# Optimization experiments

Hardware: AMD Instinct MI355X
Metric: run time of the kernel (lower is better)

Reference implementation:

```python
import jax, jax.numpy as jnp
import numpy as np

DECAY = 0.9
BETA_OBS = 1.0
BETA_STATE = 1.0

N_OBS = 20000
N_STATES = 1024
N_ACTIONS = 64
STATE_DIM = 256
RFD = 2048


def setup_inputs() -> dict:
    key = jax.random.key(0)
    ks = jax.random.split(key, 7)
    Q = jax.random.normal(ks[0], (STATE_DIM, N_STATES), dtype=jnp.float32) / np.sqrt(STATE_DIM).astype(np.float32)
    V = jax.random.normal(ks[1], (STATE_DIM, N_ACTIONS), dtype=jnp.float32) / np.sqrt(STATE_DIM).astype(np.float32)
    W = jax.random.normal(ks[2], (RFD, STATE_DIM), dtype=jnp.float32)
    M_re = jax.random.normal(ks[3], (RFD, N_OBS), dtype=jnp.float32)
    M_im = jax.random.normal(ks[4], (RFD, N_OBS), dtype=jnp.float32)
    obs = jax.random.uniform(ks[5], (N_OBS,), dtype=jnp.float32)
    action = jax.random.uniform(ks[6], (N_ACTIONS,), dtype=jnp.float32)
    return {"Q": Q, "V": V, "W": W, "M_re": M_re, "M_im": M_im, "obs": obs, "action": action}


def reference(Q, V, W, M_re, M_im, obs, action):
    # One fused POCML step: memory write (decayed outer product), state
    # rotation via complex random-feature phase, clean_up (state-kernel
    # softmax retrieval), and obs retrieval from memory.
    D = W.shape[0]  # random_feature_dim
    M = M_re + 1j * M_im                       # [D, n_obs] complex64
    obs_c = obs.astype(jnp.complex64)
    # get_state_from_memory
    state0 = M @ obs_c                         # [D]
    # update_memory: M *= decay; M += outer(state, obs)
    M_new = DECAY * M + jnp.outer(state0, obs_c)
    # update_state: v = V @ action; phi_v = exp(1j * W @ v); state *= phi_v
    v = V @ action                             # [state_dim]
    phi_v = jnp.exp(1j * (W @ v))              # [D] complex64
    state1 = state0 * phi_v
    # clean_up: phi_Q = exp(1j * W @ Q), weights = softmax(beta*sim(phi_Q.T, state))
    phi_Q = jnp.exp(1j * (W @ Q))              # [D, n_states]
    score = BETA_STATE * (phi_Q.T @ jnp.conj(state1)).real / D  # [n_states]
    weights = jax.nn.softmax(score)
    state2 = phi_Q @ weights.astype(jnp.complex64)              # [D]
    # get_obs_from_memory: softmax(beta_obs * sim(M.T, state))
    obs_score = BETA_OBS * (M_new.T @ jnp.conj(state2)).real / D  # [n_obs]
    return jax.nn.softmax(obs_score)
```

## Files before the change

kernel.cpp:

```cpp
#include <hip/hip_runtime.h>
#include <math.h>

#define N_OBS    20000
#define N_OBS4   5000
#define N_OBS8   2500
#define N_STATES 1024
#define N_ACT    64
#define SDIM     256
#define RFD      2048
#define DECAY    0.9f
#define NSEG     5
#define SEG_O8   500

typedef float v4f __attribute__((ext_vector_type(4)));
typedef float v2f __attribute__((ext_vector_type(2)));

__device__ __forceinline__ v4f ntload4(const float* p) {
    return __builtin_nontemporal_load((const v4f*)p);
}

__device__ __forceinline__ unsigned pk4_fp8(float a, float b, float c, float d) {
    unsigned w = __builtin_amdgcn_cvt_pk_fp8_f32(a, b, 0u, false);
    w = __builtin_amdgcn_cvt_pk_fp8_f32(c, d, w, true);
    return w;
}

#define OFF_SCORE  0
#define OFF_OBSACC 1024
#define ZERO_CNT   (OFF_OBSACC + N_OBS)
#define OFF_P0RE   21024
#define OFF_P0IM   (OFF_P0RE + NSEG*RFD)
#define OFF_S2RE   (OFF_P0IM + NSEG*RFD)
#define OFF_S2IM   (OFF_S2RE + RFD)
#define OFF_WTS    (OFF_S2IM + RFD)
#define OFF_VWS    (OFF_WTS + N_STATES)
#define OFF_COSQ   (OFF_VWS + SDIM)
#define OFF_SINQ   (OFF_COSQ + RFD*N_STATES)
#define OFF_MH8    (OFF_SINQ + RFD*N_STATES)
#define MH8_FLOATS (RFD * N_OBS8 * 4)
#define WS_FLOATS  (OFF_MH8 + MH8_FLOATS)

#define NB_P1     (RFD * NSEG)
#define NB_GEMM   512
#define NB_FUSED  (NB_P1 + 1 + NB_GEMM)

__global__ __launch_bounds__(256) void k_fused(
    const float* __restrict__ Mre, const float* __restrict__ Mim,
    const float* __restrict__ obs,
    const float* __restrict__ W, const float* __restrict__ Q,
    const float* __restrict__ V, const float* __restrict__ action,
    float* __restrict__ cosQ, float* __restrict__ sinQ,
    float* __restrict__ p0re, float* __restrict__ p0im,
    float* __restrict__ vout, uint4* __restrict__ Mh8)
{
    const int b = blockIdx.x;
    const int tid = threadIdx.x;

    if (b < NB_P1) {
        const int d = b / NSEG;
        const int seg = b - d * NSEG;
        const float* mr = Mre + (size_t)d * N_OBS;
        const float* mi = Mim + (size_t)d * N_OBS;
        uint4* mh = Mh8 + (size_t)d * N_OBS8;
        const float4* ob = (const float4*)obs;
        const int i0 = seg * SEG_O8;
        float ar0 = 0.f, ai0 = 0.f, ar1 = 0.f, ai1 = 0.f;
        {
            int i = i0 + tid;
            float4 oa = ob[2*i], obv = ob[2*i + 1];
            v4f ra = ntload4(mr + 8 * (size_t)i);
            v4f rb = ntload4(mr + 8 * (size_t)i + 4);
            v4f qa = ntload4(mi + 8 * (size_t)i);
            v4f qb = ntload4(mi + 8 * (size_t)i + 4);
            uint4 u;
            u.x = pk4_fp8(ra.x, qa.x, ra.y, qa.y);
            u.y = pk4_fp8(ra.z, qa.z, ra.w, qa.w);
            u.z = pk4_fp8(rb.x, qb.x, rb.y, qb.y);
            u.w = pk4_fp8(rb.z, qb.z, rb.w, qb.w);
            mh[i] = u;
            ar0 += ra.x*oa.x + ra.y*oa.y + ra.z*oa.z + ra.w*oa.w;
            ar1 += rb.x*obv.x + rb.y*obv.y + rb.z*obv.z + rb.w*obv.w;
            ai0 += qa.x*oa.x + qa.y*oa.y + qa.z*oa.z + qa.w*oa.w;
            ai1 += qb.x*obv.x + qb.y*obv.y + qb.z*obv.z + qb.w*obv.w;
        }
        if (tid < SEG_O8 - 256) {
            int i = i0 + 256 + tid;
            float4 oa = ob[2*i], obv = ob[2*i + 1];
            v4f ra = ntload4(mr + 8 * (size_t)i);
            v4f rb = ntload4(mr + 8 * (size_t)i + 4);
            v4f qa = ntload4(mi + 8 * (size_t)i);
            v4f qb = ntload4(mi + 8 * (size_t)i + 4);
            uint4 u;
            u.x = pk4_fp8(ra.x, qa.x, ra.y, qa.y);
            u.y = pk4_fp8(ra.z, qa.z, ra.w, qa.w);
            u.z = pk4_fp8(rb.x, qb.x, rb.y, qb.y);
            u.w = pk4_fp8(rb.z, qb.z, rb.w, qb.w);
            mh[i] = u;
            ar0 += ra.x*oa.x + ra.y*oa.y + ra.z*oa.z + ra.w*oa.w;
            ar1 += rb.x*obv.x + rb.y*obv.y + rb.z*obv.z + rb.w*obv.w;
            ai0 += qa.x*oa.x + qa.y*oa.y + qa.z*oa.z + qa.w*oa.w;
            ai1 += qb.x*obv.x + qb.y*obv.y + qb.z*obv.z + qb.w*obv.w;
        }
        float arr = ar0 + ar1;
        float aii = ai0 + ai1;
        #pragma unroll
        for (int off = 32; off > 0; off >>= 1) {
            arr += __shfl_down(arr, off);
            aii += __shfl_down(aii, off);
        }
        __shared__ float pr[4], pi[4];
        const int wave = tid >> 6, lane = tid & 63;
        if (lane == 0) { pr[wave] = arr; pi[wave] = aii; }
        __syncthreads();
        if (tid == 0) {
            p0re[seg * RFD + d] = pr[0] + pr[1] + pr[2] + pr[3];
            p0im[seg * RFD + d] = pi[0] + pi[1] + pi[2] + pi[3];
        }
    } else if (b == NB_P1) {
        float acc = 0.f;
        for (int a = 0; a < N_ACT; a++) acc += V[tid * N_ACT + a] * action[a];
        vout[tid] = acc;
    } else {
        const int g = b - (NB_P1 + 1);
        __shared__ float As[16][65];
        __shared__ float Bs[16][64];
        const int tx = tid & 15;
        const int ty = tid >> 4;
        const int m0 = (g >> 4) * 64;
        const int n0 = (g & 15) * 64;
        float c[4][4] = {};
        for (int k0 = 0; k0 < SDIM; k0 += 16) {
            {
                int k = tid & 15, mb = tid >> 4;
                #pragma unroll
                for (int j = 0; j < 4; j++)
                    As[k][mb + 16*j] = W[(size_t)(m0 + mb + 16*j) * SDIM + k0 + k];
            }
            {
                int n = tid & 63, kb = tid >> 6;
                #pragma unroll
                for (int j = 0; j < 4; j++)
                    Bs[kb + 4*j][n] = Q[(size_t)(k0 + kb + 4*j) * N_STATES + n0 + n];
            }
            __syncthreads();
            #pragma unroll
            for (int kk = 0; kk < 16; kk++) {
                float a[4], bb[4];
                #pragma unroll
                for (int i = 0; i < 4; i++) a[i] = As[kk][ty*4 + i];
                #pragma unroll
                for (int j = 0; j < 4; j++) bb[j] = Bs[kk][tx*4 + j];
                #pragma unroll
                for (int i = 0; i < 4; i++)
                    #pragma unroll
                    for (int j = 0; j < 4; j++)
                        c[i][j] += a[i] * bb[j];
            }
            __syncthreads();
        }
        #pragma unroll
        for (int i = 0; i < 4; i++) {
            int d = m0 + ty*4 + i;
            #pragma unroll
            for (int j = 0; j < 4; j++) {
                int s = n0 + tx*4 + j;
                float sn, cs;
                sincosf(c[i][j], &sn, &cs);
                cosQ[(size_t)d * N_STATES + s] = cs;
                sinQ[(size_t)d * N_STATES + s] = sn;
            }
        }
    }
}

__global__ __launch_bounds__(256) void k_score(
    const float* __restrict__ cosQ, const float* __restrict__ sinQ,
    const float* __restrict__ W, const float* __restrict__ vws,
    const float* __restrict__ p0re, const float* __restrict__ p0im,
    float* __restrict__ score)
{
    __shared__ float s1r_s[32], s1i_s[32];
    const int tid = threadIdx.x;
    const int d0 = blockIdx.y * 32;
    {
        const int r = tid >> 3, g = tid & 7;
        const float4* wv4 = (const float4*)(W + (size_t)(d0 + r) * SDIM + g * 32);
        const float4* vv4 = (const float4*)(vws + g * 32);
        float th = 0.f;
        #pragma unroll
        for (int j = 0; j < 8; j++) {
            float4 wv = wv4[j], vv = vv4[j];
            th += wv.x*vv.x + wv.y*vv.y + wv.z*vv.z + wv.w*vv.w;
        }
        th += __shfl_xor(th, 4);
        th += __shfl_xor(th, 2);
        th += __shfl_xor(th, 1);
        if (g == 0) {
            const int d = d0 + r;
            float re = 0.f, im = 0.f;
            #pragma unroll
            for (int s = 0; s < NSEG; s++) {
                re += p0re[s * RFD + d];
                im += p0im[s * RFD + d];
            }
            float sn, cs;
            sincosf(th, &sn, &cs);
            s1r_s[r] = re * cs - im * sn;
            s1i_s[r] = re * sn + im * cs;
        }
    }
    __syncthreads();
    const int s = blockIdx.x * 256 + tid;
    float acc = 0.f;
    #pragma unroll 4
    for (int j = 0; j < 32; j++) {
        int d = d0 + j;
        acc += cosQ[(size_t)d * N_STATES + s] * s1r_s[j]
             + sinQ[(size_t)d * N_STATES + s] * s1i_s[j];
    }
    atomicAdd(&score[s], acc);
}

__global__ __launch_bounds__(256) void k_softmax_w(
    const float* __restrict__ score, float* __restrict__ wts)
{
    __shared__ float red[256];
    const int tid = threadIdx.x;
    const float scale = 1.f / (float)RFD;
    float4 v = ((const float4*)score)[tid];
    v.x *= scale; v.y *= scale; v.z *= scale; v.w *= scale;
    float mx = fmaxf(fmaxf(v.x, v.y), fmaxf(v.z, v.w));
    red[tid] = mx; __syncthreads();
    for (int s = 128; s > 0; s >>= 1) {
        if (tid < s) red[tid] = fmaxf(red[tid], red[tid+s]);
        __syncthreads();
    }
    mx = red[0]; __syncthreads();
    float4 e;
    e.x = expf(v.x - mx); e.y = expf(v.y - mx);
    e.z = expf(v.z - mx); e.w = expf(v.w - mx);
    red[tid] = e.x + e.y + e.z + e.w; __syncthreads();
    for (int s = 128; s > 0; s >>= 1) {
        if (tid < s) red[tid] += red[tid+s];
        __syncthreads();
    }
    const float inv = 1.f / red[0];
    e.x *= inv; e.y *= inv; e.z *= inv; e.w *= inv;
    ((float4*)wts)[tid] = e;
}

__global__ __launch_bounds__(256) void k_state2(
    const float* __restrict__ cosQ, const float* __restrict__ sinQ,
    const float* __restrict__ wts,
    float* __restrict__ s2re, float* __restrict__ s2im)
{
    __shared__ float r1[256], r2[256];
    const int d = blockIdx.x, tid = threadIdx.x;
    float4 w = ((const float4*)wts)[tid];
    float4 a = ((const float4*)(cosQ + (size_t)d * N_STATES))[tid];
    float4 b = ((const float4*)(sinQ + (size_t)d * N_STATES))[tid];
    r1[tid] = a.x*w.x + a.y*w.y + a.z*w.z + a.w*w.w;
    r2[tid] = b.x*w.x + b.y*w.y + b.z*w.z + b.w*w.w;
    __syncthreads();
    for (int s = 128; s > 0; s >>= 1) {
        if (tid < s) { r1[tid] += r1[tid+s]; r2[tid] += r2[tid+s]; }
        __syncthreads();
    }
    if (tid == 0) { s2re[d] = r1[0]; s2im[d] = r2[0]; }
}

__global__ __launch_bounds__(256) void k_obs_acc8(
    const uint4* __restrict__ Mh8,
    const float* __restrict__ s2re, const float* __restrict__ s2im,
    float* __restrict__ obs_acc)
{
    __shared__ float c_s[32], s_s[32];
    const int tid = threadIdx.x;
    const int dbase = blockIdx.y * 32;
    if (tid < 32) { c_s[tid] = s2re[dbase + tid]; s_s[tid] = s2im[dbase + tid]; }
    __syncthreads();
    const int idx = blockIdx.x * 256 + tid;
    if (idx >= N_OBS8) return;
    const uint4* p = Mh8 + (size_t)dbase * N_OBS8 + idx;
    float a0 = 0.f, a1 = 0.f, a2 = 0.f, a3 = 0.f;
    float a4 = 0.f, a5 = 0.f, a6 = 0.f, a7 = 0.f;
    #pragma unroll 4
    for (int j = 0; j < 32; ++j) {
        uint4 u = p[(size_t)j * N_OBS8];
        float cc = c_s[j], ss = s_s[j];
        v2f f0 = __builtin_amdgcn_cvt_pk_f32_fp8(u.x, false);
        v2f f1 = __builtin_amdgcn_cvt_pk_f32_fp8(u.x, true);
        v2f f2 = __builtin_amdgcn_cvt_pk_f32_fp8(u.y, false);
        v2f f3 = __builtin_amdgcn_cvt_pk_f32_fp8(u.y, true);
        v2f f4 = __builtin_amdgcn_cvt_pk_f32_fp8(u.z, false);
        v2f f5 = __builtin_amdgcn_cvt_pk_f32_fp8(u.z, true);
        v2f f6 = __builtin_amdgcn_cvt_pk_f32_fp8(u.w, false);
        v2f f7 = __builtin_amdgcn_cvt_pk_f32_fp8(u.w, true);
        a0 += f0.x*cc + f0.y*ss;
        a1 += f1.x*cc + f1.y*ss;
        a2 += f2.x*cc + f2.y*ss;
        a3 += f3.x*cc + f3.y*ss;
        a4 += f4.x*cc + f4.y*ss;
        a5 += f5.x*cc + f5.y*ss;
        a6 += f6.x*cc + f6.y*ss;
        a7 += f7.x*cc + f7.y*ss;
    }
    float* dst = obs_acc + idx * 8;
    atomicAdd(dst + 0, a0);
    atomicAdd(dst + 1, a1);
    atomicAdd(dst + 2, a2);
    atomicAdd(dst + 3, a3);
    atomicAdd(dst + 4, a4);
    atomicAdd(dst + 5, a5);
    atomicAdd(dst + 6, a6);
    atomicAdd(dst + 7, a7);
}

__global__ __launch_bounds__(1024) void k_softmax_obs(
    const float* __restrict__ obs_acc, const float* __restrict__ obs,
    const float* __restrict__ p0re, const float* __restrict__ p0im,
    const float* __restrict__ s2re, const float* __restrict__ s2im,
    float* __restrict__ out)
{
    __shared__ float red[1024];
    const int tid = threadIdx.x;
    float dp = 0.f;
    #pragma unroll
    for (int i = 0; i < 2; i++) {
        int d = tid + i * 1024;
        float re = 0.f, im = 0.f;
        #pragma unroll
        for (int s = 0; s < NSEG; s++) {
            re += p0re[s * RFD + d];
            im += p0im[s * RFD + d];
        }
        dp += re * s2re[d] + im * s2im[d];
    }
    red[tid] = dp; __syncthreads();
    for (int s = 512; s > 0; s >>= 1) {
        if (tid < s) red[tid] += red[tid+s];
        __syncthreads();
    }
    const float d0 = red[0];
    __syncthreads();
    const float scale = 1.f / (float)RFD;
    float vals[20];
    float mx = -3.402823466e+38f;
    #pragma unroll
    for (int i = 0; i < 20; i++) {
        int idx = tid + i * 1024;
        if (idx < N_OBS) {
            float sc = (DECAY * obs_acc[idx] + obs[idx] * d0) * scale;
            vals[i] = sc;
            mx = fmaxf(mx, sc);
        } else vals[i] = -3.402823466e+38f;
    }
    red[tid] = mx; __syncthreads();
    for (int s = 512; s > 0; s >>= 1) {
        if (tid < s) red[tid] = fmaxf(red[tid], red[tid+s]);
        __syncthreads();
    }
    mx = red[0]; __syncthreads();
    float sum = 0.f;
    #pragma unroll
    for (int i = 0; i < 20; i++) {
        int idx = tid + i * 1024;
        if (idx < N_OBS) {
            vals[i] = expf(vals[i] - mx);
            sum += vals[i];
        }
    }
    red[tid] = sum; __syncthreads();
    for (int s = 512; s > 0; s >>= 1) {
        if (tid < s) red[tid] += red[tid+s];
        __syncthreads();
    }
    const float inv = 1.f / red[0];
    #pragma unroll
    for (int i = 0; i < 20; i++) {
        int idx = tid + i * 1024;
        if (idx < N_OBS) out[idx] = vals[i] * inv;
    }
}

extern "C" void kernel_launch(void* const* d_in, const int* in_sizes, int n_in,
                              void* d_out, int out_size, void* d_ws, size_t ws_size,
                              hipStream_t stream) {
    const float* Q      = (const float*)d_in[0];
    const float* V      = (const float*)d_in[1];
    const float* W      = (const float*)d_in[2];
    const float* Mre    = (const float*)d_in[3];
    const float* Mim    = (const float*)d_in[4];
    const float* obs    = (const float*)d_in[5];
    const float* action = (const float*)d_in[6];
    float* out = (float*)d_out;
    float* ws  = (float*)d_ws;

    if (ws_size < (size_t)WS_FLOATS * sizeof(float)) return;

    float* score = ws + OFF_SCORE;
    float* oacc  = ws + OFF_OBSACC;
    float* p0re  = ws + OFF_P0RE;
    float* p0im  = ws + OFF_P0IM;
    float* s2re  = ws + OFF_S2RE;
    float* s2im  = ws + OFF_S2IM;
    float* wts   = ws + OFF_WTS;
    float* vws   = ws + OFF_VWS;
    float* cosQ  = ws + OFF_COSQ;
    float* sinQ  = ws + OFF_SINQ;
    uint4* Mh8   = (uint4*)(ws + OFF_MH8);

    hipMemsetAsync(ws, 0, (size_t)ZERO_CNT * sizeof(float), stream);

    k_fused<<<NB_FUSED, 256, 0, stream>>>(Mre, Mim, obs, W, Q, V, action,
                                          cosQ, sinQ, p0re, p0im, vws, Mh8);
    k_score<<<dim3(4, 64), 256, 0, stream>>>(cosQ, sinQ, W, vws, p0re, p0im, score);
    k_softmax_w<<<1, 256, 0, stream>>>(score, wts);
    k_state2<<<RFD, 256, 0, stream>>>(cosQ, sinQ, wts, s2re, s2im);
    k_obs_acc8<<<dim3(10, 64), 256, 0, stream>>>(Mh8, s2re, s2im, oacc);
    k_softmax_obs<<<1, 1024, 0, stream>>>(oacc, obs, p0re, p0im, s2re, s2im, out);
}
```

Measured before the change: 444.4 us.

## Fuse softmax into state2, fold memset into fused kernel, reorder block roles

Moves workspace zeroing from a separate memset into extra blocks of the first fused kernel. The GEMM blocks are scheduled first, and the M streaming pass is split into two halves per row instead of five segments. The softmax over state scores is merged into the state2 kernel, which each block recomputes redundantly, and that kernel also reduces the state0·state2 dot product via an atomic. The aim is to save launches and the final kernel's reduction, at the cost of redundant softmax work in 1024 blocks.

```diff
diff --git a/kernel.cpp b/kernel.cpp
--- a/kernel.cpp
+++ b/kernel.cpp
@@ -2,15 +2,14 @@
 #include <math.h>
 
 #define N_OBS    20000
-#define N_OBS4   5000
 #define N_OBS8   2500
 #define N_STATES 1024
 #define N_ACT    64
 #define SDIM     256
 #define RFD      2048
 #define DECAY    0.9f
-#define NSEG     5
-#define SEG_O8   500
+#define HALF_O8  1250
+#define FLTMAX   3.402823466e+38f
 
 typedef float v4f __attribute__((ext_vector_type(4)));
 typedef float v2f __attribute__((ext_vector_type(2)));
@@ -27,22 +26,23 @@
 
 #define OFF_SCORE  0
 #define OFF_OBSACC 1024
-#define ZERO_CNT   (OFF_OBSACC + N_OBS)
-#define OFF_P0RE   21024
-#define OFF_P0IM   (OFF_P0RE + NSEG*RFD)
-#define OFF_S2RE   (OFF_P0IM + NSEG*RFD)
+#define OFF_DOT0   21024
+#define ZERO_CNT   21028
+#define OFF_P0RE   21028
+#define OFF_P0IM   (OFF_P0RE + 2*RFD)
+#define OFF_S2RE   (OFF_P0IM + 2*RFD)
 #define OFF_S2IM   (OFF_S2RE + RFD)
-#define OFF_WTS    (OFF_S2IM + RFD)
-#define OFF_VWS    (OFF_WTS + N_STATES)
+#define OFF_VWS    (OFF_S2IM + RFD)
 #define OFF_COSQ   (OFF_VWS + SDIM)
 #define OFF_SINQ   (OFF_COSQ + RFD*N_STATES)
 #define OFF_MH8    (OFF_SINQ + RFD*N_STATES)
 #define MH8_FLOATS (RFD * N_OBS8 * 4)
 #define WS_FLOATS  (OFF_MH8 + MH8_FLOATS)
 
-#define NB_P1     (RFD * NSEG)
 #define NB_GEMM   512
-#define NB_FUSED  (NB_P1 + 1 + NB_GEMM)
+#define NB_Z      21
+#define NB_P1     (RFD * 2)
+#define NB_FUSED  (NB_GEMM + 1 + NB_Z + NB_P1)
 
 __global__ __launch_bounds__(256) void k_fused(
     const float* __restrict__ Mre, const float* __restrict__ Mim,
@@ -51,83 +51,19 @@
     const float* __restrict__ V, const float* __restrict__ action,
     float* __restrict__ cosQ, float* __restrict__ sinQ,
     float* __restrict__ p0re, float* __restrict__ p0im,
-    float* __restrict__ vout, uint4* __restrict__ Mh8)
+    float* __restrict__ vout, uint4* __restrict__ Mh8,
+    float* __restrict__ zbase)
 {
     const int b = blockIdx.x;
     const int tid = threadIdx.x;
 
-    if (b < NB_P1) {
-        const int d = b / NSEG;
-        const int seg = b - d * NSEG;
-        const float* mr = Mre + (size_t)d * N_OBS;
-        const float* mi = Mim + (size_t)d * N_OBS;
-        uint4* mh = Mh8 + (size_t)d * N_OBS8;
-        const float4* ob = (const float4*)obs;
-        const int i0 = seg * SEG_O8;
-        float ar0 = 0.f, ai0 = 0.f, ar1 = 0.f, ai1 = 0.f;
-        {
-            int i = i0 + tid;
-            float4 oa = ob[2*i], obv = ob[2*i + 1];
-            v4f ra = ntload4(mr + 8 * (size_t)i);
-            v4f rb = ntload4(mr + 8 * (size_t)i + 4);
-            v4f qa = ntload4(mi + 8 * (size_t)i);
-            v4f qb = ntload4(mi + 8 * (size_t)i + 4);
-            uint4 u;
-            u.x = pk4_fp8(ra.x, qa.x, ra.y, qa.y);
-            u.y = pk4_fp8(ra.z, qa.z, ra.w, qa.w);
-            u.z = pk4_fp8(rb.x, qb.x, rb.y, qb.y);
-            u.w = pk4_fp8(rb.z, qb.z, rb.w, qb.w);
-            mh[i] = u;
-            ar0 += ra.x*oa.x + ra.y*oa.y + ra.z*oa.z + ra.w*oa.w;
-            ar1 += rb.x*obv.x + rb.y*obv.y + rb.z*obv.z + rb.w*obv.w;
-            ai0 += qa.x*oa.x + qa.y*oa.y + qa.z*oa.z + qa.w*oa.w;
-            ai1 += qb.x*obv.x + qb.y*obv.y + qb.z*obv.z + qb.w*obv.w;
-        }
-        if (tid < SEG_O8 - 256) {
-            int i = i0 + 256 + tid;
-            float4 oa = ob[2*i], obv = ob[2*i + 1];
-            v4f ra = ntload4(mr + 8 * (size_t)i);
-            v4f rb = ntload4(mr + 8 * (size_t)i + 4);
-            v4f qa = ntload4(mi + 8 * (size_t)i);
-            v4f qb = ntload4(mi + 8 * (size_t)i + 4);
-            uint4 u;
-            u.x = pk4_fp8(ra.x, qa.x, ra.y, qa.y);
-            u.y = pk4_fp8(ra.z, qa.z, ra.w, qa.w);
-            u.z = pk4_fp8(rb.x, qb.x, rb.y, qb.y);
-            u.w = pk4_fp8(rb.z, qb.z, rb.w, qb.w);
-            mh[i] = u;
-            ar0 += ra.x*oa.x + ra.y*oa.y + ra.z*oa.z + ra.w*oa.w;
-            ar1 += rb.x*obv.x + rb.y*obv.y + rb.z*obv.z + rb.w*obv.w;
-            ai0 += qa.x*oa.x + qa.y*oa.y + qa.z*oa.z + qa.w*oa.w;
-            ai1 += qb.x*obv.x + qb.y*obv.y + qb.z*obv.z + qb.w*obv.w;
-        }
-        float arr = ar0 + ar1;
-        float aii = ai0 + ai1;
-        #pragma unroll
-        for (int off = 32; off > 0; off >>= 1) {
-            arr += __shfl_down(arr, off);
-            aii += __shfl_down(aii, off);
-        }
-        __shared__ float pr[4], pi[4];
-        const int wave = tid >> 6, lane = tid & 63;
-        if (lane == 0) { pr[wave] = arr; pi[wave] = aii; }
-        __syncthreads();
-        if (tid == 0) {
-            p0re[seg * RFD + d] = pr[0] + pr[1] + pr[2] + pr[3];
-            p0im[seg * RFD + d] = pi[0] + pi[1] + pi[2] + pi[3];
-        }
-    } else if (b == NB_P1) {
-        float acc = 0.f;
-        for (int a = 0; a < N_ACT; a++) acc += V[tid * N_ACT + a] * action[a];
-        vout[tid] = acc;
-    } else {
-        const int g = b - (NB_P1 + 1);
+    if (b < NB_GEMM) {
         __shared__ float As[16][65];
         __shared__ float Bs[16][64];
         const int tx = tid & 15;
         const int ty = tid >> 4;
-        const int m0 = (g >> 4) * 64;
-        const int n0 = (g & 15) * 64;
+        const int m0 = (b >> 4) * 64;
+        const int n0 = (b & 15) * 64;
         float c[4][4] = {};
         for (int k0 = 0; k0 < SDIM; k0 += 16) {
             {
@@ -170,6 +106,61 @@
                 sinQ[(size_t)d * N_STATES + s] = sn;
             }
         }
+    } else if (b == NB_GEMM) {
+        float acc = 0.f;
+        for (int a = 0; a < N_ACT; a++) acc += V[tid * N_ACT + a] * action[a];
+        vout[tid] = acc;
+    } else if (b < NB_GEMM + 1 + NB_Z) {
+        int idx = (b - (NB_GEMM + 1)) * 256 + tid;
+        if (idx < ZERO_CNT / 4)
+            ((float4*)zbase)[idx] = make_float4(0.f, 0.f, 0.f, 0.f);
+    } else {
+        const int p = b - (NB_GEMM + 1 + NB_Z);
+        const int d = p >> 1;
+        const int h = p & 1;
+        const float* mr = Mre + (size_t)d * N_OBS;
+        const float* mi = Mim + (size_t)d * N_OBS;
+        uint4* mh = Mh8 + (size_t)d * N_OBS8;
+        const float4* ob = (const float4*)obs;
+        const int base = h * HALF_O8, lim = base + HALF_O8;
+        float ar0 = 0.f, ar1 = 0.f, ai0 = 0.f, ai1 = 0.f;
+        int i = base + tid;
+        #pragma unroll
+        for (int it = 0; it < 5; ++it, i += 256) {
+            int ic = i < lim ? i : lim - 1;
+            float4 oa = ob[2*ic], obv = ob[2*ic + 1];
+            v4f ra = ntload4(mr + 8 * (size_t)ic);
+            v4f rb = ntload4(mr + 8 * (size_t)ic + 4);
+            v4f qa = ntload4(mi + 8 * (size_t)ic);
+            v4f qb = ntload4(mi + 8 * (size_t)ic + 4);
+            if (i < lim) {
+                uint4 u;
+                u.x = pk4_fp8(ra.x, qa.x, ra.y, qa.y);
+                u.y = pk4_fp8(ra.z, qa.z, ra.w, qa.w);
+                u.z = pk4_fp8(rb.x, qb.x, rb.y, qb.y);
+                u.w = pk4_fp8(rb.z, qb.z, rb.w, qb.w);
+                mh[ic] = u;
+                ar0 += ra.x*oa.x + ra.y*oa.y + ra.z*oa.z + ra.w*oa.w;
+                ar1 += rb.x*obv.x + rb.y*obv.y + rb.z*obv.z + rb.w*obv.w;
+                ai0 += qa.x*oa.x + qa.y*oa.y + qa.z*oa.z + qa.w*oa.w;
+                ai1 += qb.x*obv.x + qb.y*obv.y + qb.z*obv.z + qb.w*obv.w;
+            }
+        }
+        float arr = ar0 + ar1;
+        float aii = ai0 + ai1;
+        #pragma unroll
+        for (int off = 32; off > 0; off >>= 1) {
+            arr += __shfl_down(arr, off);
+            aii += __shfl_down(aii, off);
+        }
+        __shared__ float pr[4], pi[4];
+        const int wave = tid >> 6, lane = tid & 63;
+        if (lane == 0) { pr[wave] = arr; pi[wave] = aii; }
+        __syncthreads();
+        if (tid == 0) {
+            p0re[h * RFD + d] = pr[0] + pr[1] + pr[2] + pr[3];
+            p0im[h * RFD + d] = pi[0] + pi[1] + pi[2] + pi[3];
+        }
     }
 }
 
@@ -197,12 +188,8 @@
         th += __shfl_xor(th, 1);
         if (g == 0) {
             const int d = d0 + r;
-            float re = 0.f, im = 0.f;
-            #pragma unroll
-            for (int s = 0; s < NSEG; s++) {
-                re += p0re[s * RFD + d];
-                im += p0im[s * RFD + d];
-            }
+            float re = p0re[d] + p0re[RFD + d];
+            float im = p0im[d] + p0im[RFD + d];
             float sn, cs;
             sincosf(th, &sn, &cs);
             s1r_s[r] = re * cs - im * sn;
@@ -221,10 +208,16 @@
     atomicAdd(&score[s], acc);
 }
 
-__global__ __launch_bounds__(256) void k_softmax_w(
-    const float* __restrict__ score, float* __restrict__ wts)
+__global__ __launch_bounds__(256) void k_wst2(
+    const float* __restrict__ cosQ, const float* __restrict__ sinQ,
+    const float* __restrict__ score,
+    const float* __restrict__ p0re, const float* __restrict__ p0im,
+    float* __restrict__ s2re, float* __restrict__ s2im,
+    float* __restrict__ dot0)
 {
     __shared__ float red[256];
+    __shared__ float r1[256], r2[256];
+    const int b = blockIdx.x;
     const int tid = threadIdx.x;
     const float scale = 1.f / (float)RFD;
     float4 v = ((const float4*)score)[tid];
@@ -246,27 +239,29 @@
     }
     const float inv = 1.f / red[0];
     e.x *= inv; e.y *= inv; e.z *= inv; e.w *= inv;
-    ((float4*)wts)[tid] = e;
-}
-
-__global__ __launch_bounds__(256) void k_state2(
-    const float* __restrict__ cosQ, const float* __restrict__ sinQ,
-    const float* __restrict__ wts,
-    float* __restrict__ s2re, float* __restrict__ s2im)
-{
-    __shared__ float r1[256], r2[256];
-    const int d = blockIdx.x, tid = threadIdx.x;
-    float4 w = ((const float4*)wts)[tid];
-    float4 a = ((const float4*)(cosQ + (size_t)d * N_STATES))[tid];
-    float4 b = ((const float4*)(sinQ + (size_t)d * N_STATES))[tid];
-    r1[tid] = a.x*w.x + a.y*w.y + a.z*w.z + a.w*w.w;
-    r2[tid] = b.x*w.x + b.y*w.y + b.z*w.z + b.w*w.w;
     __syncthreads();
-    for (int s = 128; s > 0; s >>= 1) {
-        if (tid < s) { r1[tid] += r1[tid+s]; r2[tid] += r2[tid+s]; }
-        __syncthreads();
-    }
-    if (tid == 0) { s2re[d] = r1[0]; s2im[d] = r2[0]; }
+    float blockdot = 0.f;
+    #pragma unroll
+    for (int r = 0; r < 2; r++) {
+        const int d = b * 2 + r;
+        float4 a = ((const float4*)(cosQ + (size_t)d * N_STATES))[tid];
+        float4 bb = ((const float4*)(sinQ + (size_t)d * N_STATES))[tid];
+        r1[tid] = a.x*e.x + a.y*e.y + a.z*e.z + a.w*e.w;
+        r2[tid] = bb.x*e.x + bb.y*e.y + bb.z*e.z + bb.w*e.w;
+        __syncthreads();
+        for (int s = 128; s > 0; s >>= 1) {
+            if (tid < s) { r1[tid] += r1[tid+s]; r2[tid] += r2[tid+s]; }
+            __syncthreads();
+        }
+        if (tid == 0) {
+            s2re[d] = r1[0]; s2im[d] = r2[0];
+            float s0r = p0re[d] + p0re[RFD + d];
+            float s0i = p0im[d] + p0im[RFD + d];
+            blockdot += s0r * r1[0] + s0i * r2[0];
+        }
+        __syncthreads();
+    }
+    if (tid == 0) atomicAdd(dot0, blockdot);
 }
 
 __global__ __launch_bounds__(256) void k_obs_acc8(
@@ -318,34 +313,15 @@
 
 __global__ __launch_bounds__(1024) void k_softmax_obs(
     const float* __restrict__ obs_acc, const float* __restrict__ obs,
-    const float* __restrict__ p0re, const float* __restrict__ p0im,
-    const float* __restrict__ s2re, const float* __restrict__ s2im,
+    const float* __restrict__ dot0,
     float* __restrict__ out)
 {
     __shared__ float red[1024];
     const int tid = threadIdx.x;
-    float dp = 0.f;
-    #pragma unroll
-    for (int i = 0; i < 2; i++) {
-        int d = tid + i * 1024;
-        float re = 0.f, im = 0.f;
-        #pragma unroll
-        for (int s = 0; s < NSEG; s++) {
-            re += p0re[s * RFD + d];
-            im += p0im[s * RFD + d];
-        }
-        dp += re * s2re[d] + im * s2im[d];
-    }
-    red[tid] = dp; __syncthreads();
-    for (int s = 512; s > 0; s >>= 1) {
-        if (tid < s) red[tid] += red[tid+s];
-        __syncthreads();
-    }
-    const float d0 = red[0];
-    __syncthreads();
+    const float d0 = dot0[0];
     const float scale = 1.f / (float)RFD;
     float vals[20];
-    float mx = -3.402823466e+38f;
+    float mx = -FLTMAX;
     #pragma unroll
     for (int i = 0; i < 20; i++) {
         int idx = tid + i * 1024;
@@ -353,7 +329,7 @@
             float sc = (DECAY * obs_acc[idx] + obs[idx] * d0) * scale;
             vals[i] = sc;
             mx = fmaxf(mx, sc);
-        } else vals[i] = -3.402823466e+38f;
+        } else vals[i] = -FLTMAX;
     }
     red[tid] = mx; __syncthreads();
     for (int s = 512; s > 0; s >>= 1) {
@@ -400,23 +376,21 @@
 
     float* score = ws + OFF_SCORE;
     float* oacc  = ws + OFF_OBSACC;
+    float* dot0  = ws + OFF_DOT0;
     float* p0re  = ws + OFF_P0RE;
     float* p0im  = ws + OFF_P0IM;
     float* s2re  = ws + OFF_S2RE;
     float* s2im  = ws + OFF_S2IM;
-    float* wts   = ws + OFF_WTS;
     float* vws   = ws + OFF_VWS;
     float* cosQ  = ws + OFF_COSQ;
     float* sinQ  = ws + OFF_SINQ;
     uint4* Mh8   = (uint4*)(ws + OFF_MH8);
 
-    hipMemsetAsync(ws, 0, (size_t)ZERO_CNT * sizeof(float), stream);
-
     k_fused<<<NB_FUSED, 256, 0, stream>>>(Mre, Mim, obs, W, Q, V, action,
-                                          cosQ, sinQ, p0re, p0im, vws, Mh8);
+                                          cosQ, sinQ, p0re, p0im, vws, Mh8, ws);
     k_score<<<dim3(4, 64), 256, 0, stream>>>(cosQ, sinQ, W, vws, p0re, p0im, score);
-    k_softmax_w<<<1, 256, 0, stream>>>(score, wts);
-    k_state2<<<RFD, 256, 0, stream>>>(cosQ, sinQ, wts, s2re, s2im);
+    k_wst2<<<RFD / 2, 256, 0, stream>>>(cosQ, sinQ, score, p0re, p0im,
+                                        s2re, s2im, dot0);
     k_obs_acc8<<<dim3(10, 64), 256, 0, stream>>>(Mh8, s2re, s2im, oacc);
-    k_softmax_obs<<<1, 1024, 0, stream>>>(oacc, obs, p0re, p0im, s2re, s2im, out);
-}
+    k_softmax_obs<<<1, 1024, 0, stream>>>(oacc, obs, dot0, out);
+}
```

Measured after the change: 440.4 us. Within noise of the previous version (-0.9%).
